# Optimization experiments

Measured on AMD Instinct MI355X. Metric: run time of the kernel, lower is better.

## Reference

```python
import math
import jax, jax.numpy as jnp
import numpy as np

N_EXPERTS = 8
CAP_FACTOR = 1.25
D_MODEL = 1024
D_FF = 4096
B, T = 8, 2048


def setup_inputs() -> dict:
    key = jax.random.key(0)
    k1, k2, k3, k4 = jax.random.split(key, 4)
    hidden = jax.random.normal(k1, (B, T, D_MODEL), dtype=jnp.float32)
    # router: Linear(d_model, n_experts, bias=False), init std=0.01; store as (D, E)
    router_w = jax.random.normal(k2, (D_MODEL, N_EXPERTS), dtype=jnp.float32) * 0.01
    # per-expert MLP weights stacked: W1 (E, D, F), W2 (E, F, D)
    s1 = 1.0 / math.sqrt(D_MODEL)
    s2 = 1.0 / math.sqrt(D_FF)
    W1 = jax.random.uniform(k3, (N_EXPERTS, D_MODEL, D_FF), dtype=jnp.float32, minval=-s1, maxval=s1)
    W2 = jax.random.uniform(k4, (N_EXPERTS, D_FF, D_MODEL), dtype=jnp.float32, minval=-s2, maxval=s2)
    return {"hidden": hidden, "router_w": router_w, "W1": W1, "W2": W2}


def reference(hidden, router_w, W1, W2):
    Bb, Tt, D = hidden.shape
    N = Bb * Tt
    E = router_w.shape[1]
    capacity = min(int(math.ceil(CAP_FACTOR * N / E)), N)

    hidden_flat = hidden.reshape(N, D)
    logits = hidden_flat @ router_w                 # (N, E)
    router_probs = jax.nn.softmax(logits, axis=-1)  # (N, E)

    scores = router_probs.T                         # (E, N)
    weights, indices = jax.lax.top_k(scores, capacity)  # (E, C) each

    # gather tokens per expert: (E, C, D)
    expert_in = hidden_flat[indices]
    h = jnp.einsum('ecd,edf->ecf', expert_in, W1)
    h = jax.nn.gelu(h, approximate=False)           # torch nn.GELU default (erf)
    expert_out = jnp.einsum('ecf,efd->ecd', h, W2)  # (E, C, D)
    contrib = weights[..., None] * expert_out       # (E, C, D)

    output = jnp.zeros((N, D), dtype=hidden.dtype)
    output = output.at[indices.reshape(-1)].add(contrib.reshape(-1, D))
    output = output.reshape(Bb, Tt, D)

    eps = 1e-8
    entropy = -(router_probs * jnp.log(router_probs + eps)).sum(-1)
    aux_loss = -entropy.mean()
    return output, aux_loss
```

## Files before the change

### kernel.cpp

```cpp
#include <hip/hip_runtime.h>
#include <hip/hip_bf16.h>
#include <math.h>

#define NTOK 16384
#define DM 1024
#define DFF 4096
#define NEXP 8
#define CAP 2560

typedef __bf16 bf16;
typedef float f32x4 __attribute__((ext_vector_type(4)));
typedef bf16 bf16x8 __attribute__((ext_vector_type(8)));
typedef bf16 bf16x4 __attribute__((ext_vector_type(4)));

#define OFF_PROBS 0ull
#define OFF_IDX   524288ull
#define OFF_WTS   606208ull
#define OFF_W1T   688128ull
#define OFF_W2T   67796992ull
#define OFF_X     134905856ull
#define OFF_ENT   OFF_X
#define OFF_H     176848896ull
#define WS_MIN    197820416ull
#define WS_FUSED  344621056ull

#define BAR() do { asm volatile("" ::: "memory"); __builtin_amdgcn_s_barrier(); asm volatile("" ::: "memory"); } while (0)

__device__ __forceinline__ void gl16(const bf16* g, const bf16* l) {
  __builtin_amdgcn_global_load_lds((const __attribute__((address_space(1))) void*)g,
                                   (__attribute__((address_space(3))) void*)l, 16, 0, 0);
}

__device__ __forceinline__ float gelu_f(float x) {
  float u = 1.5957691216057308f * (x + 0.044715f * x * x * x);
  return x / (1.f + __expf(-u));
}

__global__ __launch_bounds__(256) void k_transpose_cvt(const float* __restrict__ src,
                                                       bf16* __restrict__ dst, int R, int C) {
  __shared__ float tile[64][69];
  int e = blockIdx.z;
  src += (size_t)e * R * C;
  dst += (size_t)e * R * C;
  int c0 = blockIdx.x * 64, r0 = blockIdx.y * 64;
  int t = threadIdx.x;
  int tr = t >> 4, tc4 = (t & 15) * 4;
#pragma unroll
  for (int i = 0; i < 4; i++) {
    int r = tr + i * 16;
    float4 v = *(const float4*)(src + (size_t)(r0 + r) * C + c0 + tc4);
    tile[r][tc4] = v.x; tile[r][tc4 + 1] = v.y; tile[r][tc4 + 2] = v.z; tile[r][tc4 + 3] = v.w;
  }
  __syncthreads();
#pragma unroll
  for (int i = 0; i < 4; i++) {
    int orr = tr + i * 16;
    bf16x4 o = {(bf16)tile[tc4][orr], (bf16)tile[tc4 + 1][orr],
                (bf16)tile[tc4 + 2][orr], (bf16)tile[tc4 + 3][orr]};
    *(bf16x4*)(dst + (size_t)(c0 + orr) * R + r0 + tc4) = o;
  }
}

__global__ __launch_bounds__(256) void k_router(const float* __restrict__ hidden,
                                                const float* __restrict__ rw,
                                                float* __restrict__ probsT,
                                                float* __restrict__ entPart) {
  __shared__ float went[4];
  int wv = threadIdx.x >> 6, lane = threadIdx.x & 63;
  int token = blockIdx.x * 4 + wv;
  float acc[NEXP];
#pragma unroll
  for (int e = 0; e < NEXP; e++) acc[e] = 0.f;
  const float* hp = hidden + (size_t)token * DM;
  for (int d = lane; d < DM; d += 64) {
    float h = hp[d];
#pragma unroll
    for (int e = 0; e < NEXP; e++) acc[e] = fmaf(h, rw[d * NEXP + e], acc[e]);
  }
#pragma unroll
  for (int e = 0; e < NEXP; e++) {
    float v = acc[e];
#pragma unroll
    for (int s = 1; s < 64; s <<= 1) v += __shfl_xor(v, s);
    acc[e] = v;
  }
  float mx = acc[0];
#pragma unroll
  for (int e = 1; e < NEXP; e++) mx = fmaxf(mx, acc[e]);
  float p[NEXP], s = 0.f;
#pragma unroll
  for (int e = 0; e < NEXP; e++) { p[e] = expf(acc[e] - mx); s += p[e]; }
  float inv = 1.f / s;
  float ent = 0.f;
#pragma unroll
  for (int e = 0; e < NEXP; e++) { p[e] *= inv; ent += p[e] * logf(p[e] + 1e-8f); }
  if (lane < NEXP) probsT[(size_t)lane * NTOK + token] = p[lane];
  if (lane == 0) went[wv] = ent;
  __syncthreads();
  if (threadIdx.x == 0) entPart[blockIdx.x] = went[0] + went[1] + went[2] + went[3];
}

__global__ __launch_bounds__(256) void k_aux(const float* __restrict__ part, float* __restrict__ outAux) {
  __shared__ float s[256];
  int t = threadIdx.x;
  float v = 0.f;
#pragma unroll
  for (int i = 0; i < 16; i++) v += part[i * 256 + t];
  s[t] = v;
  __syncthreads();
  for (int st = 128; st > 0; st >>= 1) {
    if (t < st) s[t] += s[t + st];
    __syncthreads();
  }
  if (t == 0) outAux[0] = s[0] * (1.f / (float)NTOK);
}

__global__ __launch_bounds__(1024) void k_topk(const float* __restrict__ probsT,
                                               int* __restrict__ idx,
                                               float* __restrict__ wts) {
  int e = blockIdx.x;
  const float* row = probsT + (size_t)e * NTOK;
  int t = threadIdx.x;
  unsigned u[16];
#pragma unroll
  for (int j = 0; j < 16; j++) u[j] = __float_as_uint(row[j * 1024 + t]);
  __shared__ int wred[16];
  __shared__ int bc;
  __shared__ int cnt_gt, cnt_eq;
  __shared__ int eqbuf[2048];
  int lane = t & 63, wv = t >> 6;
  unsigned prefix = 0;
  for (int bit = 30; bit >= 0; bit--) {
    unsigned cand = prefix | (1u << bit);
    int c = 0;
#pragma unroll
    for (int j = 0; j < 16; j++) c += (u[j] >= cand) ? 1 : 0;
#pragma unroll
    for (int s = 1; s < 64; s <<= 1) c += __shfl_xor(c, s);
    if (lane == 0) wred[wv] = c;
    __syncthreads();
    if (t == 0) { int tot = 0; for (int k = 0; k < 16; k++) tot += wred[k]; bc = tot; }
    __syncthreads();
    if (bc >= CAP) prefix = cand;
  }
  unsigned vC = prefix;
  if (t == 0) { cnt_gt = 0; cnt_eq = 0; }
  __syncthreads();
#pragma unroll
  for (int j = 0; j < 16; j++) {
    int i = j * 1024 + t;
    if (u[j] > vC) {
      int p = atomicAdd(&cnt_gt, 1);
      idx[e * CAP + p] = i;
      wts[e * CAP + p] = __uint_as_float(u[j]);
    } else if (u[j] == vC) {
      int p = atomicAdd(&cnt_eq, 1);
      if (p < 2048) eqbuf[p] = i;
    }
  }
  __syncthreads();
  int m = cnt_gt;
  int ne = cnt_eq > 2048 ? 2048 : cnt_eq;
  int needed = CAP - m;
  for (int j = t; j < ne; j += 1024) {
    int my = eqbuf[j];
    int rank = 0;
    for (int k = 0; k < ne; k++) rank += (eqbuf[k] < my) ? 1 : 0;
    if (rank < needed) {
      idx[e * CAP + m + rank] = my;
      wts[e * CAP + m + rank] = __uint_as_float(vC);
    }
  }
}

__global__ void k_gather(const float* __restrict__ hidden, const int* __restrict__ idx,
                         bf16* __restrict__ X) {
  int ec = blockIdx.x;
  int token = idx[ec];
  const float4* src = (const float4*)(hidden + (size_t)token * DM);
  bf16* dstrow = X + (size_t)ec * DM;
  int t = threadIdx.x;
  float4 v = src[t];
  bf16x4 o = {(bf16)v.x, (bf16)v.y, (bf16)v.z, (bf16)v.w};
  *(bf16x4*)(dstrow + t * 4) = o;
}

template <int EPI>
__global__ __launch_bounds__(512, 2) void k_gemm256(
    const bf16* __restrict__ Ab, const bf16* __restrict__ Bb,
    bf16* __restrict__ Hb, const int* __restrict__ idxb, const float* __restrict__ wtsb,
    float* __restrict__ outb, int zOffset) {
  constexpr int KD  = (EPI == 0) ? DM : DFF;
  constexpr int NBX = 10;
  constexpr int NBY = (EPI == 0) ? 16 : 4;
  constexpr int NT  = (EPI == 0) ? 16 : 32;

  __shared__ bf16 As[2][256 * 64];
  __shared__ bf16 Bs[2][256 * 64];

  int nwg = gridDim.x;
  int wg = (blockIdx.x & 7) * (nwg >> 3) + (blockIdx.x >> 3);
  int zl = wg / (NBX * NBY);
  int r = wg % (NBX * NBY);
  int by = r % NBY, bx = r / NBY;
  int z = zl + zOffset;
  int e, k0;
  const bf16 *A, *B;
  if constexpr (EPI == 0) {
    e = z; k0 = 0;
    A = Ab + (size_t)e * CAP * DM;
    B = Bb + (size_t)e * DFF * DM;
  } else {
    e = z >> 1; k0 = (z & 1) * (DFF / 2);
    A = Ab + (size_t)e * CAP * DFF;
    B = Bb + (size_t)e * DM * DFF;
  }
  int m0 = bx * 256, n0 = by * 256;

  int t = threadIdx.x, lane = t & 63, wv = t >> 6;
  int wm = wv >> 2, wn = wv & 3;
  int l3 = lane >> 3, l7 = lane & 7;
  int cswz = (l7 ^ l3) * 8;

  auto stage = [&](int half, int ktE, int buf) {
#pragma unroll
    for (int j = 0; j < 2; ++j) {
      int u = wv * 2 + j;
      int rb;
      const bf16* G;
      bf16* L;
      if (half == 0) { rb = u * 8 + (u >> 3) * 64;       G = A + (size_t)(m0 + rb + l3) * KD; L = &As[buf][rb * 64]; }
      else if (half == 3) { rb = 64 + u * 8 + (u >> 3) * 64; G = A + (size_t)(m0 + rb + l3) * KD; L = &As[buf][rb * 64]; }
      else if (half == 1) { rb = (u >> 2) * 64 + (u & 3) * 8;      G = B + (size_t)(n0 + rb + l3) * KD; L = &Bs[buf][rb * 64]; }
      else { rb = (u >> 2) * 64 + 32 + (u & 3) * 8; G = B + (size_t)(n0 + rb + l3) * KD; L = &Bs[buf][rb * 64]; }
      gl16(G + ktE + cswz, L + lane * 8);
    }
  };

  auto rdA = [&](const bf16* base, int q, int i, int kk) -> bf16x8 {
    int rr = wm * 128 + (q * 4 + i) * 16 + (lane & 15);
    int slot = (kk * 4 + (lane >> 4)) ^ l7;
    return *(const bf16x8*)((const char*)base + rr * 128 + slot * 16);
  };
  auto rdB = [&](const bf16* base, int h, int i, int kk) -> bf16x8 {
    int rr = wn * 64 + (h * 2 + i) * 16 + (lane & 15);
    int slot = (kk * 4 + (lane >> 4)) ^ l7;
    return *(const bf16x8*)((const char*)base + rr * 128 + slot * 16);
  };

  f32x4 acc[8][4];
#pragma unroll
  for (int m = 0; m < 8; m++)
#pragma unroll
    for (int n = 0; n < 4; n++) acc[m][n] = (f32x4){0.f, 0.f, 0.f, 0.f};
  bf16x8 aF[4][2], bF0[2][2], bF1[2][2];

  stage(0, k0, 0); stage(1, k0, 0); stage(2, k0, 0); stage(3, k0, 0);
  asm volatile("s_waitcnt vmcnt(4)" ::: "memory");
  BAR();

  for (int kt = 0; kt < NT; ++kt) {
    int cur = kt & 1;
    int nxE = k0 + (kt + 1) * 64;
    bool nl = (kt < NT - 1);
#pragma unroll
    for (int i = 0; i < 4; i++)
#pragma unroll
      for (int kk = 0; kk < 2; kk++) aF[i][kk] = rdA(As[cur], 0, i, kk);
#pragma unroll
    for (int i = 0; i < 2; i++)
#pragma unroll
      for (int kk = 0; kk < 2; kk++) bF0[i][kk] = rdB(Bs[cur], 0, i, kk);
    if (nl) stage(0, nxE, cur ^ 1);
    BAR();
    asm volatile("s_waitcnt lgkmcnt(0)" ::: "memory");
    __builtin_amdgcn_s_setprio(1);
#pragma unroll
    for (int i = 0; i < 4; i++)
#pragma unroll
      for (int j = 0; j < 2; j++)
#pragma unroll
        for (int kk = 0; kk < 2; kk++)
          acc[i][j] = __builtin_amdgcn_mfma_f32_16x16x32_bf16(aF[i][kk], bF0[j][kk], acc[i][j], 0, 0, 0);
    __builtin_amdgcn_s_setprio(0);
    if (nl) asm volatile("s_waitcnt vmcnt(4)" ::: "memory");
    else    asm volatile("s_waitcnt vmcnt(2)" ::: "memory");
    BAR();
#pragma unroll
    for (int i = 0; i < 2; i++)
#pragma unroll
      for (int kk = 0; kk < 2; kk++) bF1[i][kk] = rdB(Bs[cur], 1, i, kk);
    if (nl) stage(1, nxE, cur ^ 1);
    BAR();
    asm volatile("s_waitcnt lgkmcnt(0)" ::: "memory");
    __builtin_amdgcn_s_setprio(1);
#pragma unroll
    for (int i = 0; i < 4; i++)
#pragma unroll
      for (int j = 0; j < 2; j++)
#pragma unroll
        for (int kk = 0; kk < 2; kk++)
          acc[i][2 + j] = __builtin_amdgcn_mfma_f32_16x16x32_bf16(aF[i][kk], bF1[j][kk], acc[i][2 + j], 0, 0, 0);
    __builtin_amdgcn_s_setprio(0);
    if (nl) asm volatile("s_waitcnt vmcnt(4)" ::: "memory");
    else    asm volatile("s_waitcnt vmcnt(0)" ::: "memory");
    BAR();
#pragma unroll
    for (int i = 0; i < 4; i++)
#pragma unroll
      for (int kk = 0; kk < 2; kk++) aF[i][kk] = rdA(As[cur], 1, i, kk);
    if (nl) stage(2, nxE, cur ^ 1);
    BAR();
    asm volatile("s_waitcnt lgkmcnt(0)" ::: "memory");
    __builtin_amdgcn_s_setprio(1);
#pragma unroll
    for (int i = 0; i < 4; i++)
#pragma unroll
      for (int j = 0; j < 2; j++)
#pragma unroll
        for (int kk = 0; kk < 2; kk++)
          acc[4 + i][j] = __builtin_amdgcn_mfma_f32_16x16x32_bf16(aF[i][kk], bF0[j][kk], acc[4 + i][j], 0, 0, 0);
    __builtin_amdgcn_s_setprio(0);
    BAR();
    if (nl) stage(3, nxE, cur ^ 1);
    BAR();
    __builtin_amdgcn_s_setprio(1);
#pragma unroll
    for (int i = 0; i < 4; i++)
#pragma unroll
      for (int j = 0; j < 2; j++)
#pragma unroll
        for (int kk = 0; kk < 2; kk++)
          acc[4 + i][2 + j] = __builtin_amdgcn_mfma_f32_16x16x32_bf16(aF[i][kk], bF1[j][kk], acc[4 + i][2 + j], 0, 0, 0);
    __builtin_amdgcn_s_setprio(0);
    if (nl) asm volatile("s_waitcnt vmcnt(4)" ::: "memory");
    BAR();
  }

  int cl = lane & 15, rg = (lane >> 4) * 4;
  if constexpr (EPI == 0) {
    bf16* He = Hb + (size_t)e * CAP * DFF;
#pragma unroll
    for (int m = 0; m < 8; m++) {
      int rowg = m0 + wm * 128 + m * 16 + rg;
#pragma unroll
      for (int n = 0; n < 4; n++) {
        int col = n0 + wn * 64 + n * 16 + cl;
#pragma unroll
        for (int rr = 0; rr < 4; rr++)
          He[(size_t)(rowg + rr) * DFF + col] = (bf16)gelu_f(acc[m][n][rr]);
      }
    }
  } else {
    const int* idxE = idxb + e * CAP;
    const float* wtsE = wtsb + e * CAP;
#pragma unroll
    for (int m = 0; m < 8; m++) {
      int rowg = m0 + wm * 128 + m * 16 + rg;
#pragma unroll
      for (int rr = 0; rr < 4; rr++) {
        int c = rowg + rr;
        int token = idxE[c];
        float w = wtsE[c];
        float* op = outb + (size_t)token * DM + n0 + wn * 64 + cl;
#pragma unroll
        for (int n = 0; n < 4; n++) atomicAdd(op + n * 16, w * acc[m][n][rr]);
      }
    }
  }
}

extern "C" void kernel_launch(void* const* d_in, const int* in_sizes, int n_in,
                              void* d_out, int out_size, void* d_ws, size_t ws_size,
                              hipStream_t stream) {
  const float* hidden = (const float*)d_in[0];
  const float* router_w = (const float*)d_in[1];
  const float* W1 = (const float*)d_in[2];
  const float* W2 = (const float*)d_in[3];
  float* out = (float*)d_out;
  if (ws_size < WS_MIN) return;

  char* ws = (char*)d_ws;
  float* probsT = (float*)(ws + OFF_PROBS);
  int* idxb = (int*)(ws + OFF_IDX);
  float* wtsb = (float*)(ws + OFF_WTS);
  bf16* W1T = (bf16*)(ws + OFF_W1T);
  bf16* W2T = (bf16*)(ws + OFF_W2T);
  bf16* Xall = (bf16*)(ws + OFF_X);
  float* entPart = (float*)(ws + OFF_ENT);
  bf16* Hbuf = (bf16*)(ws + OFF_H);

  hipMemsetAsync(d_out, 0, (size_t)out_size * sizeof(float), stream);

  k_transpose_cvt<<<dim3(DFF / 64, DM / 64, NEXP), 256, 0, stream>>>(W1, W1T, DM, DFF);
  k_transpose_cvt<<<dim3(DM / 64, DFF / 64, NEXP), 256, 0, stream>>>(W2, W2T, DFF, DM);

  k_router<<<NTOK / 4, 256, 0, stream>>>(hidden, router_w, probsT, entPart);
  k_aux<<<1, 256, 0, stream>>>(entPart, out + (size_t)NTOK * DM);
  k_topk<<<NEXP, 1024, 0, stream>>>(probsT, idxb, wtsb);
  k_gather<<<NEXP * CAP, 256, 0, stream>>>(hidden, idxb, Xall);

  if (ws_size >= WS_FUSED) {
    k_gemm256<0><<<1280, 512, 0, stream>>>(Xall, W1T, Hbuf, nullptr, nullptr, nullptr, 0);
    k_gemm256<1><<<640, 512, 0, stream>>>(Hbuf, W2T, nullptr, idxb, wtsb, out, 0);
  } else {
    for (int e = 0; e < NEXP; e++) {
      bf16* Hadj = Hbuf - (size_t)e * CAP * DFF;
      k_gemm256<0><<<160, 512, 0, stream>>>(Xall, W1T, Hadj, nullptr, nullptr, nullptr, e);
      k_gemm256<1><<<80, 512, 0, stream>>>(Hadj, W2T, nullptr, idxb, wtsb, out, e * 2);
    }
  }
}
```

Before: 667.0 us.

## Make expert GEMMs persistent with cross-tile prefetch of next tile's first K-slice

Replaces the one-tile-per-workgroup GEMM launches with a persistent grid of 256 workgroups. Each workgroup is pinned to one expert and walks several 256x256 output tiles, and on the last K step it prefetches the first K slice of its next tile, so the pipeline does not drain between tiles. This aims to remove the tail and wave-quantization overhead and the pipeline ramp-up cost of the many-block launches. It leaves an uneven per-workgroup tile count in the second GEMM (3 vs 2 tiles) and adds an accumulator reset between tiles. GELU also switches its division to a fast reciprocal.

```diff
diff --git a/kernel.cpp b/kernel.cpp
--- a/kernel.cpp
+++ b/kernel.cpp
@@ -33,7 +33,7 @@
 
 __device__ __forceinline__ float gelu_f(float x) {
   float u = 1.5957691216057308f * (x + 0.044715f * x * x * x);
-  return x / (1.f + __expf(-u));
+  return x * __builtin_amdgcn_rcpf(1.f + __expf(-u));
 }
 
 __global__ __launch_bounds__(256) void k_transpose_cvt(const float* __restrict__ src,
@@ -186,66 +186,61 @@
 }
 
 template <int EPI>
-__global__ __launch_bounds__(512, 2) void k_gemm256(
+__global__ __launch_bounds__(512, 2) void k_gemm256p(
     const bf16* __restrict__ Ab, const bf16* __restrict__ Bb,
     bf16* __restrict__ Hb, const int* __restrict__ idxb, const float* __restrict__ wtsb,
-    float* __restrict__ outb, int zOffset) {
-  constexpr int KD  = (EPI == 0) ? DM : DFF;
-  constexpr int NBX = 10;
-  constexpr int NBY = (EPI == 0) ? 16 : 4;
-  constexpr int NT  = (EPI == 0) ? 16 : 32;
+    float* __restrict__ outb, int serialE) {
+  constexpr int KD = (EPI == 0) ? DM : DFF;
+  constexpr int NT = (EPI == 0) ? 16 : 32;
 
   __shared__ bf16 As[2][256 * 64];
   __shared__ bf16 Bs[2][256 * 64];
 
-  int nwg = gridDim.x;
-  int wg = (blockIdx.x & 7) * (nwg >> 3) + (blockIdx.x >> 3);
-  int zl = wg / (NBX * NBY);
-  int r = wg % (NBX * NBY);
-  int by = r % NBY, bx = r / NBY;
-  int z = zl + zOffset;
-  int e, k0;
-  const bf16 *A, *B;
-  if constexpr (EPI == 0) {
-    e = z; k0 = 0;
-    A = Ab + (size_t)e * CAP * DM;
-    B = Bb + (size_t)e * DFF * DM;
-  } else {
-    e = z >> 1; k0 = (z & 1) * (DFF / 2);
-    A = Ab + (size_t)e * CAP * DFF;
-    B = Bb + (size_t)e * DM * DFF;
-  }
-  int m0 = bx * 256, n0 = by * 256;
+  int e, slot, nA;
+  if (serialE >= 0) { e = serialE; slot = blockIdx.x; nA = 1; }
+  else {
+    e = blockIdx.x & 7;
+    slot = blockIdx.x >> 3;
+    nA = (EPI == 0) ? 5 : ((slot < 16) ? 3 : 2);
+  }
+  const bf16* A = Ab + (size_t)e * ((EPI == 0) ? (size_t)CAP * DM : (size_t)CAP * DFF);
+  const bf16* B = Bb + (size_t)e * ((EPI == 0) ? (size_t)DFF * DM : (size_t)DM * DFF);
 
   int t = threadIdx.x, lane = t & 63, wv = t >> 6;
   int wm = wv >> 2, wn = wv & 3;
   int l3 = lane >> 3, l7 = lane & 7;
   int cswz = (l7 ^ l3) * 8;
 
-  auto stage = [&](int half, int ktE, int buf) {
+  auto decode = [&](int seq, int& m0, int& n0, int& k0) {
+    int s_ = seq / 40, r_ = seq % 40;
+    int bx = r_ >> 2, q = r_ & 3;
+    m0 = bx * 256;
+    if constexpr (EPI == 0) { n0 = (s_ * 4 + q) * 256; k0 = 0; }
+    else { n0 = q * 256; k0 = s_ * 2048; }
+  };
+
+  auto stage = [&](const bf16* Am, const bf16* Bn, int half, int ktE, int buf) {
 #pragma unroll
     for (int j = 0; j < 2; ++j) {
       int u = wv * 2 + j;
-      int rb;
-      const bf16* G;
-      bf16* L;
-      if (half == 0) { rb = u * 8 + (u >> 3) * 64;       G = A + (size_t)(m0 + rb + l3) * KD; L = &As[buf][rb * 64]; }
-      else if (half == 3) { rb = 64 + u * 8 + (u >> 3) * 64; G = A + (size_t)(m0 + rb + l3) * KD; L = &As[buf][rb * 64]; }
-      else if (half == 1) { rb = (u >> 2) * 64 + (u & 3) * 8;      G = B + (size_t)(n0 + rb + l3) * KD; L = &Bs[buf][rb * 64]; }
-      else { rb = (u >> 2) * 64 + 32 + (u & 3) * 8; G = B + (size_t)(n0 + rb + l3) * KD; L = &Bs[buf][rb * 64]; }
+      int rb; const bf16* G; bf16* L;
+      if (half == 0)      { rb = u * 8 + (u >> 3) * 64;            G = Am + (size_t)(rb + l3) * KD; L = &As[buf][rb * 64]; }
+      else if (half == 3) { rb = 64 + u * 8 + (u >> 3) * 64;       G = Am + (size_t)(rb + l3) * KD; L = &As[buf][rb * 64]; }
+      else if (half == 1) { rb = (u >> 2) * 64 + (u & 3) * 8;      G = Bn + (size_t)(rb + l3) * KD; L = &Bs[buf][rb * 64]; }
+      else                { rb = (u >> 2) * 64 + 32 + (u & 3) * 8; G = Bn + (size_t)(rb + l3) * KD; L = &Bs[buf][rb * 64]; }
       gl16(G + ktE + cswz, L + lane * 8);
     }
   };
 
   auto rdA = [&](const bf16* base, int q, int i, int kk) -> bf16x8 {
     int rr = wm * 128 + (q * 4 + i) * 16 + (lane & 15);
-    int slot = (kk * 4 + (lane >> 4)) ^ l7;
-    return *(const bf16x8*)((const char*)base + rr * 128 + slot * 16);
+    int slt = (kk * 4 + (lane >> 4)) ^ l7;
+    return *(const bf16x8*)((const char*)base + rr * 128 + slt * 16);
   };
   auto rdB = [&](const bf16* base, int h, int i, int kk) -> bf16x8 {
     int rr = wn * 64 + (h * 2 + i) * 16 + (lane & 15);
-    int slot = (kk * 4 + (lane >> 4)) ^ l7;
-    return *(const bf16x8*)((const char*)base + rr * 128 + slot * 16);
+    int slt = (kk * 4 + (lane >> 4)) ^ l7;
+    return *(const bf16x8*)((const char*)base + rr * 128 + slt * 16);
   };
 
   f32x4 acc[8][4];
@@ -255,118 +250,145 @@
     for (int n = 0; n < 4; n++) acc[m][n] = (f32x4){0.f, 0.f, 0.f, 0.f};
   bf16x8 aF[4][2], bF0[2][2], bF1[2][2];
 
-  stage(0, k0, 0); stage(1, k0, 0); stage(2, k0, 0); stage(3, k0, 0);
+  int seq = slot;
+  int m0, n0, k0;
+  decode(seq, m0, n0, k0);
+  const bf16* Am = A + (size_t)m0 * KD;
+  const bf16* Bn = B + (size_t)n0 * KD;
+
+  stage(Am, Bn, 0, k0, 0); stage(Am, Bn, 1, k0, 0);
+  stage(Am, Bn, 2, k0, 0); stage(Am, Bn, 3, k0, 0);
   asm volatile("s_waitcnt vmcnt(4)" ::: "memory");
   BAR();
 
-  for (int kt = 0; kt < NT; ++kt) {
-    int cur = kt & 1;
-    int nxE = k0 + (kt + 1) * 64;
-    bool nl = (kt < NT - 1);
-#pragma unroll
-    for (int i = 0; i < 4; i++)
-#pragma unroll
-      for (int kk = 0; kk < 2; kk++) aF[i][kk] = rdA(As[cur], 0, i, kk);
-#pragma unroll
-    for (int i = 0; i < 2; i++)
-#pragma unroll
-      for (int kk = 0; kk < 2; kk++) bF0[i][kk] = rdB(Bs[cur], 0, i, kk);
-    if (nl) stage(0, nxE, cur ^ 1);
-    BAR();
-    asm volatile("s_waitcnt lgkmcnt(0)" ::: "memory");
-    __builtin_amdgcn_s_setprio(1);
-#pragma unroll
-    for (int i = 0; i < 4; i++)
-#pragma unroll
-      for (int j = 0; j < 2; j++)
-#pragma unroll
-        for (int kk = 0; kk < 2; kk++)
-          acc[i][j] = __builtin_amdgcn_mfma_f32_16x16x32_bf16(aF[i][kk], bF0[j][kk], acc[i][j], 0, 0, 0);
-    __builtin_amdgcn_s_setprio(0);
-    if (nl) asm volatile("s_waitcnt vmcnt(4)" ::: "memory");
-    else    asm volatile("s_waitcnt vmcnt(2)" ::: "memory");
-    BAR();
-#pragma unroll
-    for (int i = 0; i < 2; i++)
-#pragma unroll
-      for (int kk = 0; kk < 2; kk++) bF1[i][kk] = rdB(Bs[cur], 1, i, kk);
-    if (nl) stage(1, nxE, cur ^ 1);
-    BAR();
-    asm volatile("s_waitcnt lgkmcnt(0)" ::: "memory");
-    __builtin_amdgcn_s_setprio(1);
-#pragma unroll
-    for (int i = 0; i < 4; i++)
-#pragma unroll
-      for (int j = 0; j < 2; j++)
-#pragma unroll
-        for (int kk = 0; kk < 2; kk++)
-          acc[i][2 + j] = __builtin_amdgcn_mfma_f32_16x16x32_bf16(aF[i][kk], bF1[j][kk], acc[i][2 + j], 0, 0, 0);
-    __builtin_amdgcn_s_setprio(0);
-    if (nl) asm volatile("s_waitcnt vmcnt(4)" ::: "memory");
-    else    asm volatile("s_waitcnt vmcnt(0)" ::: "memory");
-    BAR();
-#pragma unroll
-    for (int i = 0; i < 4; i++)
-#pragma unroll
-      for (int kk = 0; kk < 2; kk++) aF[i][kk] = rdA(As[cur], 1, i, kk);
-    if (nl) stage(2, nxE, cur ^ 1);
-    BAR();
-    asm volatile("s_waitcnt lgkmcnt(0)" ::: "memory");
-    __builtin_amdgcn_s_setprio(1);
-#pragma unroll
-    for (int i = 0; i < 4; i++)
-#pragma unroll
-      for (int j = 0; j < 2; j++)
-#pragma unroll
-        for (int kk = 0; kk < 2; kk++)
-          acc[4 + i][j] = __builtin_amdgcn_mfma_f32_16x16x32_bf16(aF[i][kk], bF0[j][kk], acc[4 + i][j], 0, 0, 0);
-    __builtin_amdgcn_s_setprio(0);
-    BAR();
-    if (nl) stage(3, nxE, cur ^ 1);
-    BAR();
-    __builtin_amdgcn_s_setprio(1);
-#pragma unroll
-    for (int i = 0; i < 4; i++)
-#pragma unroll
-      for (int j = 0; j < 2; j++)
-#pragma unroll
-        for (int kk = 0; kk < 2; kk++)
-          acc[4 + i][2 + j] = __builtin_amdgcn_mfma_f32_16x16x32_bf16(aF[i][kk], bF1[j][kk], acc[4 + i][2 + j], 0, 0, 0);
-    __builtin_amdgcn_s_setprio(0);
-    if (nl) asm volatile("s_waitcnt vmcnt(4)" ::: "memory");
-    BAR();
-  }
-
-  int cl = lane & 15, rg = (lane >> 4) * 4;
-  if constexpr (EPI == 0) {
-    bf16* He = Hb + (size_t)e * CAP * DFF;
-#pragma unroll
-    for (int m = 0; m < 8; m++) {
-      int rowg = m0 + wm * 128 + m * 16 + rg;
-#pragma unroll
-      for (int n = 0; n < 4; n++) {
-        int col = n0 + wn * 64 + n * 16 + cl;
-#pragma unroll
-        for (int rr = 0; rr < 4; rr++)
-          He[(size_t)(rowg + rr) * DFF + col] = (bf16)gelu_f(acc[m][n][rr]);
+  for (int a = 0; a < nA; ++a) {
+    int m0N = 0, n0N = 0, k0N = 0;
+    const bf16 *AmN = nullptr, *BnN = nullptr;
+    bool hasNextA = (a + 1 < nA);
+    if (hasNextA) {
+      decode(seq + 32, m0N, n0N, k0N);
+      AmN = A + (size_t)m0N * KD;
+      BnN = B + (size_t)n0N * KD;
+    }
+    for (int kt = 0; kt < NT; ++kt) {
+      int cur = kt & 1;
+      bool lastT = (kt == NT - 1);
+      bool nl = !lastT || hasNextA;
+      const bf16* sA = lastT ? AmN : Am;
+      const bf16* sB = lastT ? BnN : Bn;
+      int sk = lastT ? k0N : (k0 + (kt + 1) * 64);
+
+#pragma unroll
+      for (int i = 0; i < 4; i++)
+#pragma unroll
+        for (int kk = 0; kk < 2; kk++) aF[i][kk] = rdA(As[cur], 0, i, kk);
+#pragma unroll
+      for (int i = 0; i < 2; i++)
+#pragma unroll
+        for (int kk = 0; kk < 2; kk++) bF0[i][kk] = rdB(Bs[cur], 0, i, kk);
+      if (nl) stage(sA, sB, 0, sk, cur ^ 1);
+      BAR();
+      asm volatile("s_waitcnt lgkmcnt(0)" ::: "memory");
+      __builtin_amdgcn_s_setprio(1);
+#pragma unroll
+      for (int i = 0; i < 4; i++)
+#pragma unroll
+        for (int j = 0; j < 2; j++)
+#pragma unroll
+          for (int kk = 0; kk < 2; kk++)
+            acc[i][j] = __builtin_amdgcn_mfma_f32_16x16x32_bf16(aF[i][kk], bF0[j][kk], acc[i][j], 0, 0, 0);
+      __builtin_amdgcn_s_setprio(0);
+      if (nl) asm volatile("s_waitcnt vmcnt(4)" ::: "memory");
+      else    asm volatile("s_waitcnt vmcnt(2)" ::: "memory");
+      BAR();
+#pragma unroll
+      for (int i = 0; i < 2; i++)
+#pragma unroll
+        for (int kk = 0; kk < 2; kk++) bF1[i][kk] = rdB(Bs[cur], 1, i, kk);
+      if (nl) stage(sA, sB, 1, sk, cur ^ 1);
+      BAR();
+      asm volatile("s_waitcnt lgkmcnt(0)" ::: "memory");
+      __builtin_amdgcn_s_setprio(1);
+#pragma unroll
+      for (int i = 0; i < 4; i++)
+#pragma unroll
+        for (int j = 0; j < 2; j++)
+#pragma unroll
+          for (int kk = 0; kk < 2; kk++)
+            acc[i][2 + j] = __builtin_amdgcn_mfma_f32_16x16x32_bf16(aF[i][kk], bF1[j][kk], acc[i][2 + j], 0, 0, 0);
+      __builtin_amdgcn_s_setprio(0);
+      if (nl) asm volatile("s_waitcnt vmcnt(4)" ::: "memory");
+      else    asm volatile("s_waitcnt vmcnt(0)" ::: "memory");
+      BAR();
+#pragma unroll
+      for (int i = 0; i < 4; i++)
+#pragma unroll
+        for (int kk = 0; kk < 2; kk++) aF[i][kk] = rdA(As[cur], 1, i, kk);
+      if (nl) stage(sA, sB, 2, sk, cur ^ 1);
+      BAR();
+      asm volatile("s_waitcnt lgkmcnt(0)" ::: "memory");
+      __builtin_amdgcn_s_setprio(1);
+#pragma unroll
+      for (int i = 0; i < 4; i++)
+#pragma unroll
+        for (int j = 0; j < 2; j++)
+#pragma unroll
+          for (int kk = 0; kk < 2; kk++)
+            acc[4 + i][j] = __builtin_amdgcn_mfma_f32_16x16x32_bf16(aF[i][kk], bF0[j][kk], acc[4 + i][j], 0, 0, 0);
+      __builtin_amdgcn_s_setprio(0);
+      BAR();
+      if (nl) stage(sA, sB, 3, sk, cur ^ 1);
+      BAR();
+      __builtin_amdgcn_s_setprio(1);
+#pragma unroll
+      for (int i = 0; i < 4; i++)
+#pragma unroll
+        for (int j = 0; j < 2; j++)
+#pragma unroll
+          for (int kk = 0; kk < 2; kk++)
+            acc[4 + i][2 + j] = __builtin_amdgcn_mfma_f32_16x16x32_bf16(aF[i][kk], bF1[j][kk], acc[4 + i][2 + j], 0, 0, 0);
+      __builtin_amdgcn_s_setprio(0);
+      if (nl) asm volatile("s_waitcnt vmcnt(4)" ::: "memory");
+      BAR();
+    }
+
+    int cl = lane & 15, rg = (lane >> 4) * 4;
+    if constexpr (EPI == 0) {
+      bf16* He = Hb + (size_t)e * CAP * DFF;
+#pragma unroll
+      for (int m = 0; m < 8; m++) {
+        int rowg = m0 + wm * 128 + m * 16 + rg;
+#pragma unroll
+        for (int n = 0; n < 4; n++) {
+          int col = n0 + wn * 64 + n * 16 + cl;
+#pragma unroll
+          for (int rr = 0; rr < 4; rr++)
+            He[(size_t)(rowg + rr) * DFF + col] = (bf16)gelu_f(acc[m][n][rr]);
+        }
       }
-    }
-  } else {
-    const int* idxE = idxb + e * CAP;
-    const float* wtsE = wtsb + e * CAP;
-#pragma unroll
-    for (int m = 0; m < 8; m++) {
-      int rowg = m0 + wm * 128 + m * 16 + rg;
-#pragma unroll
-      for (int rr = 0; rr < 4; rr++) {
-        int c = rowg + rr;
-        int token = idxE[c];
-        float w = wtsE[c];
-        float* op = outb + (size_t)token * DM + n0 + wn * 64 + cl;
-#pragma unroll
-        for (int n = 0; n < 4; n++) atomicAdd(op + n * 16, w * acc[m][n][rr]);
+    } else {
+      const int* idxE = idxb + e * CAP;
+      const float* wtsE = wtsb + e * CAP;
+#pragma unroll
+      for (int m = 0; m < 8; m++) {
+        int rowg = m0 + wm * 128 + m * 16 + rg;
+#pragma unroll
+        for (int rr = 0; rr < 4; rr++) {
+          int c = rowg + rr;
+          int token = idxE[c];
+          float w = wtsE[c];
+          float* op = outb + (size_t)token * DM + n0 + wn * 64 + cl;
+#pragma unroll
+          for (int n = 0; n < 4; n++) atomicAdd(op + n * 16, w * acc[m][n][rr]);
+        }
       }
     }
+#pragma unroll
+    for (int m = 0; m < 8; m++)
+#pragma unroll
+      for (int n = 0; n < 4; n++) acc[m][n] = (f32x4){0.f, 0.f, 0.f, 0.f};
+
+    if (hasNextA) { m0 = m0N; n0 = n0N; k0 = k0N; Am = AmN; Bn = BnN; seq += 32; }
   }
 }
 
@@ -401,13 +423,13 @@
   k_gather<<<NEXP * CAP, 256, 0, stream>>>(hidden, idxb, Xall);
 
   if (ws_size >= WS_FUSED) {
-    k_gemm256<0><<<1280, 512, 0, stream>>>(Xall, W1T, Hbuf, nullptr, nullptr, nullptr, 0);
-    k_gemm256<1><<<640, 512, 0, stream>>>(Hbuf, W2T, nullptr, idxb, wtsb, out, 0);
+    k_gemm256p<0><<<256, 512, 0, stream>>>(Xall, W1T, Hbuf, nullptr, nullptr, nullptr, -1);
+    k_gemm256p<1><<<256, 512, 0, stream>>>(Hbuf, W2T, nullptr, idxb, wtsb, out, -1);
   } else {
     for (int e = 0; e < NEXP; e++) {
       bf16* Hadj = Hbuf - (size_t)e * CAP * DFF;
-      k_gemm256<0><<<160, 512, 0, stream>>>(Xall, W1T, Hadj, nullptr, nullptr, nullptr, e);
-      k_gemm256<1><<<80, 512, 0, stream>>>(Hadj, W2T, nullptr, idxb, wtsb, out, e * 2);
-    }
-  }
-}
+      k_gemm256p<0><<<160, 512, 0, stream>>>(Xall, W1T, Hadj, nullptr, nullptr, nullptr, e);
+      k_gemm256p<1><<<80, 512, 0, stream>>>(Hadj, W2T, nullptr, idxb, wtsb, out, e);
+    }
+  }
+}
```

Measured after the change: 671.1 us. No clear change (+0.6%).
